# Kernel tuning notes

Hardware: AMD Instinct MI355X
Metric: run time of the kernel (lower is better)

## Reference

```python
import jax, jax.numpy as jnp
import numpy as np

N, E, IN, H, OUT, G = 100000, 1600000, 9, 64, 6, 1024
EPS = 1e-5


def setup_inputs() -> dict:
    key = jax.random.key(0)
    ks = jax.random.split(key, 24)
    inp = {
        "x": jax.random.normal(ks[0], (N, IN), dtype=jnp.float32),
        "edge_index": jax.random.randint(ks[1], (2, E), 0, N, dtype=jnp.int64),
        "edge_weight": jax.random.uniform(ks[2], (E,), dtype=jnp.float32),
        "batch": jnp.sort(jax.random.randint(ks[3], (N,), 0, G, dtype=jnp.int64)),
    }
    def lin(k, fan_in, fan_out):
        return jax.random.normal(k, (fan_in, fan_out), dtype=jnp.float32) / np.sqrt(fan_in)
    # GraphConv layer 0: IN -> H; layers 1,2: H -> H
    inp["W_rel0"], inp["W_root0"], inp["b0"] = lin(ks[4], IN, H), lin(ks[5], IN, H), jnp.zeros((H,), jnp.float32)
    inp["W_rel1"], inp["W_root1"], inp["b1"] = lin(ks[6], H, H), lin(ks[7], H, H), jnp.zeros((H,), jnp.float32)
    inp["W_rel2"], inp["W_root2"], inp["b2"] = lin(ks[8], H, H), lin(ks[9], H, H), jnp.zeros((H,), jnp.float32)
    # BatchNorm params for the first num_layers-1 = 2 layers
    inp["g0"], inp["be0"] = jnp.ones((H,), jnp.float32), jnp.zeros((H,), jnp.float32)
    inp["g1"], inp["be1"] = jnp.ones((H,), jnp.float32), jnp.zeros((H,), jnp.float32)
    # MLP head
    inp["W_l1"], inp["b_l1"] = lin(ks[10], H, H), jnp.zeros((H,), jnp.float32)
    inp["W_l2"], inp["b_l2"] = lin(ks[11], H, OUT), jnp.zeros((OUT,), jnp.float32)
    return inp


def graph_conv(x, src, dst, ew, W_rel, W_root, b):
    # PyG GraphConv: out = aggr_add(e_ji * x_j) @ W_rel + b + x @ W_root
    msg = x[src] * ew[:, None]                      # [E, F] gather
    agg = jax.ops.segment_sum(msg, dst, num_segments=x.shape[0])  # [N, F] scatter-add
    return agg @ W_rel + b + x @ W_root


def batch_norm(x, g, b):
    m = jnp.mean(x, axis=0)
    v = jnp.var(x, axis=0)
    return (x - m) * jax.lax.rsqrt(v + EPS) * g + b


def reference(x, edge_index, edge_weight, batch,
              W_rel0, W_root0, b0, W_rel1, W_root1, b1, W_rel2, W_root2, b2,
              g0, be0, g1, be1, W_l1, b_l1, W_l2, b_l2):
    src, dst = edge_index[0], edge_index[1]
    # layer 0: conv -> BN -> relu (dropout p applied only in training; eval here)
    h = graph_conv(x, src, dst, edge_weight, W_rel0, W_root0, b0)
    h = jax.nn.relu(batch_norm(h, g0, be0))
    # layer 1
    h = graph_conv(h, src, dst, edge_weight, W_rel1, W_root1, b1)
    h = jax.nn.relu(batch_norm(h, g1, be1))
    # layer 2 (no norm/relu)
    h = graph_conv(h, src, dst, edge_weight, W_rel2, W_root2, b2)
    # global mean pool over graphs
    summed = jax.ops.segment_sum(h, batch, num_segments=G)            # [G, H]
    counts = jax.ops.segment_sum(jnp.ones((h.shape[0],), h.dtype), batch, num_segments=G)
    pooled = summed / jnp.maximum(counts, 1.0)[:, None]
    # MLP head
    z = jax.nn.relu(pooled @ W_l1 + b_l1)
    return z @ W_l2 + b_l2
```

## Files before the change

kernel.cpp:

```cpp
#include <hip/hip_runtime.h>
#include <hip/hip_fp16.h>

constexpr int N    = 100000;
constexpr int E    = 1600000;
constexpr int FIN  = 9;
constexpr int OUTF = 6;
constexpr int G    = 1024;
constexpr int NPB  = 256;
constexpr int NB   = (N + NPB - 1) / NPB;
constexpr int CH   = 2048;
constexpr int NCH  = (E + CH - 1) / CH;
constexpr int BCAP = 4864;
constexpr int CBCAP= BCAP + NPB + 8;
constexpr int EBUF = 5888;
constexpr int ZCNT = 256 + G * 64;

typedef _Float16 f16x8 __attribute__((ext_vector_type(8)));
typedef float    f32x4 __attribute__((ext_vector_type(4)));

__device__ __forceinline__ void atomAddF(float* p, float v) { unsafeAtomicAdd(p, v); }

__global__ __launch_bounds__(256) void initK(int* __restrict__ cursor, float* __restrict__ zeros,
    const float* __restrict__ x, __half* __restrict__ x9)
{
    int i = blockIdx.x * 256 + threadIdx.x;
    if (i < NB) cursor[i] = i * BCAP;
    if (i < ZCNT) zeros[i] = 0.f;
    if (i < N * FIN) x9[i] = __float2half(x[i]);
}

__global__ __launch_bounds__(256) void passA(const int* __restrict__ src, const int* __restrict__ dst,
    const float* __restrict__ ew, int* __restrict__ cursor, int2* __restrict__ bucketed)
{
    __shared__ int h[NB];
    __shared__ int hb[NB];
    int t = threadIdx.x;
    for (int i = t; i < NB; i += 256) h[i] = 0;
    __syncthreads();
    int base = blockIdx.x * CH;
    int myS[8], myD[8], rk[8]; float myW[8];
#pragma unroll
    for (int i = 0; i < 8; i++) {
        int e = base + i * 256 + t;
        if (e < E) {
            myS[i] = src[e]; myD[i] = dst[e]; myW[i] = ew[e];
            rk[i] = atomicAdd(&h[myD[i] >> 8], 1);
        } else myD[i] = -1;
    }
    __syncthreads();
    for (int i = t; i < NB; i += 256) hb[i] = h[i] ? atomicAdd(&cursor[i], h[i]) : 0;
    __syncthreads();
#pragma unroll
    for (int i = 0; i < 8; i++) if (myD[i] >= 0) {
        int packed = myS[i] | ((myD[i] & 255) << 24);
        bucketed[hb[myD[i] >> 8] + rk[i]] = make_int2(packed, __float_as_int(myW[i]));
    }
}

__global__ __launch_bounds__(NPB) void passB(const int* __restrict__ cursor,
    const int2* __restrict__ bucketed, int* __restrict__ ebeg, int* __restrict__ eend,
    int2* __restrict__ csr)
{
    __shared__ int2 ebuf[EBUF];
    __shared__ int cl[NPB], sa[NPB], sb[NPB], curs[NPB];
    int b = blockIdx.x, t = threadIdx.x;
    int node0 = b * NPB;
    int nnode = min(NPB, N - node0);
    int cnt = cursor[b] - b * BCAP;
    int abase = b * BCAP;
    int base = b * CBCAP;
    bool fits = (cnt <= EBUF);
    cl[t] = 0;
    __syncthreads();
    for (int e = t; e < cnt; e += NPB) {
        int2 r = bucketed[abase + e];
        if (fits) ebuf[e] = r;
        atomicAdd(&cl[((unsigned)r.x) >> 24], 1);
    }
    __syncthreads();
    int deg = cl[t];
    int pc = (deg + 1) & ~1;
    int* cur = sa; int* nxt = sb;
    cur[t] = pc;
    __syncthreads();
    for (int o = 1; o < NPB; o <<= 1) {
        int v = cur[t];
        if (t >= o) v += cur[t - o];
        nxt[t] = v;
        __syncthreads();
        int* tmp = cur; cur = nxt; nxt = tmp;
    }
    int off = cur[t] - pc;
    if (t < nnode) { ebeg[node0 + t] = base + off; eend[node0 + t] = base + off + deg; }
    curs[t] = off;
    __syncthreads();
    for (int e = t; e < cnt; e += NPB) {
        int2 r = fits ? ebuf[e] : bucketed[abase + e];
        int dl = ((unsigned)r.x) >> 24;
        int pos = base + atomicAdd(&curs[dl], 1);
        csr[pos] = make_int2(r.x & 0x00FFFFFF, r.y);
    }
    __syncthreads();
    if (t < nnode && (deg & 1)) csr[base + off + deg] = make_int2(0, 0);
    if (t < 4) csr[base + cur[NPB - 1] + t] = make_int2(0, 0);
}

__global__ __launch_bounds__(256) void wprep(const float* __restrict__ Wrel1, const float* __restrict__ Wroot1,
    const float* __restrict__ Wrel2, const float* __restrict__ Wroot2, __half* __restrict__ Wt)
{
    int i = blockIdx.x * 256 + threadIdx.x;
    int layer = i >> 13, r = i & 8191;
    int c = r >> 6, k = r & 63;
    const float* Wrel = layer ? Wrel2 : Wrel1;
    const float* Wroot = layer ? Wroot2 : Wroot1;
    float v = (c < 64) ? Wrel[k * 64 + c] : Wroot[k * 64 + (c - 64)];
    Wt[i] = __float2half(v);
}

__global__ __launch_bounds__(256) void gather9(const __half* __restrict__ x9,
    const int2* __restrict__ csr, const int* __restrict__ ebeg, const int* __restrict__ eend,
    float* __restrict__ agg9)
{
    int t = threadIdx.x, lane = t & 63;
    int es = lane >> 4, fc = min(lane & 15, FIN - 1);
    int wv = (blockIdx.x * blockDim.x + t) >> 6;
    int nw = (gridDim.x * blockDim.x) >> 6;
    for (int n = wv; n < N; n += nw) {
        int beg = ebeg[n], end = eend[n];
        int last = end - 1;
        int2 eA0 = csr[min(beg + es,      last)];
        int2 eB0 = csr[min(beg + 4 + es,  last)];
        int2 eA1 = csr[min(beg + 8 + es,  last)];
        int2 eB1 = csr[min(beg + 12 + es, last)];
        __half xA = x9[(size_t)eA0.x * FIN + fc];
        __half xB = x9[(size_t)eB0.x * FIN + fc];
        float a0 = 0.f, a1 = 0.f;
        for (int k = beg; k < end; k += 8) {
            int2 eA2 = csr[min(k + 16 + es, last)];
            int2 eB2 = csr[min(k + 20 + es, last)];
            __half nxA = x9[(size_t)eA1.x * FIN + fc];
            __half nxB = x9[(size_t)eB1.x * FIN + fc];
            float wA = (k + es     < end) ? __int_as_float(eA0.y) : 0.f;
            float wB = (k + 4 + es < end) ? __int_as_float(eB0.y) : 0.f;
            a0 = fmaf(wA, __half2float(xA), a0);
            a1 = fmaf(wB, __half2float(xB), a1);
            eA0 = eA1; eB0 = eB1; eA1 = eA2; eB1 = eB2;
            xA = nxA; xB = nxB;
        }
        float r = a0 + a1;
        r += __shfl(r, lane ^ 16, 64);
        r += __shfl(r, lane ^ 32, 64);
        if (lane < FIN) agg9[(size_t)n * FIN + lane] = r;
    }
}

__global__ __launch_bounds__(256) void proj0post(const float* __restrict__ x,
    const float* __restrict__ agg9, const float* __restrict__ Wrel,
    const float* __restrict__ Wroot, const float* __restrict__ bias,
    __half* __restrict__ H0, float* __restrict__ stats)
{
    int t = threadIdx.x, j = t & 63;
    int nl = __builtin_amdgcn_readfirstlane(t >> 6);
    float wrel[FIN], wroot[FIN];
#pragma unroll
    for (int k = 0; k < FIN; k++) { wrel[k] = Wrel[k * 64 + j]; wroot[k] = Wroot[k * 64 + j]; }
    float bj = bias[j];
    float s1 = 0.f, s2 = 0.f;
    const int ntiles = N / 4;
    for (int tile = blockIdx.x; tile < ntiles; tile += gridDim.x) {
        int n = tile * 4 + nl;
        const float* xr = x + (size_t)n * FIN;
        const float* ar = agg9 + (size_t)n * FIN;
        float acc = bj;
#pragma unroll
        for (int k = 0; k < FIN; k++) {
            acc = fmaf(ar[k], wrel[k], acc);
            acc = fmaf(xr[k], wroot[k], acc);
        }
        H0[(size_t)n * 64 + j] = __float2half(acc);
        s1 += acc; s2 += acc * acc;
    }
    __shared__ float sred[256];
    sred[t] = s1; __syncthreads();
    if (t < 64) atomAddF(&stats[t], sred[t] + sred[t+64] + sred[t+128] + sred[t+192]);
    __syncthreads();
    sred[t] = s2; __syncthreads();
    if (t < 64) atomAddF(&stats[64 + t], sred[t] + sred[t+64] + sred[t+128] + sred[t+192]);
}

__global__ __launch_bounds__(256) void projm(const __half* __restrict__ Hin, const __half* __restrict__ Wt,
    const float* __restrict__ bias, const float* __restrict__ stats,
    const float* __restrict__ gam, const float* __restrict__ bet,
    __half* __restrict__ P, __half* __restrict__ Hout)
{
    int t = threadIdx.x, lane = t & 63;
    int wv = blockIdx.x * 4 + (t >> 6);
    int nw = gridDim.x * 4;
    int n16 = lane & 15, quad = lane >> 4;
    constexpr float invN = 1.0f / (float)N;
    float sc[16], sh[16];
#pragma unroll
    for (int jj = 0; jj < 16; jj++) {
        int k = (jj < 8) ? (quad * 8 + jj) : (32 + quad * 8 + (jj - 8));
        float m = stats[k] * invN;
        float v = stats[64 + k] * invN - m * m;
        sc[jj] = gam[k] * rsqrtf(v + 1e-5f);
        sh[jj] = bet[k] - m * sc[jj];
    }
    f16x8 bf[8][2];
#pragma unroll
    for (int ct = 0; ct < 8; ct++)
#pragma unroll
        for (int kh = 0; kh < 2; kh++)
            bf[ct][kh] = *(const f16x8*)(Wt + (size_t)(ct * 16 + n16) * 64 + kh * 32 + quad * 8);
    float bcol[4];
#pragma unroll
    for (int i = 0; i < 4; i++) bcol[i] = bias[i * 16 + n16];
    const int NT = N / 16;
    for (int tile = wv; tile < NT; tile += nw) {
        int n0 = tile * 16;
        f16x8 r0 = *(const f16x8*)(Hin + (size_t)(n0 + n16) * 64 + quad * 8);
        f16x8 r1 = *(const f16x8*)(Hin + (size_t)(n0 + n16) * 64 + 32 + quad * 8);
        f16x8 a0, a1;
#pragma unroll
        for (int jj = 0; jj < 8; jj++) {
            a0[jj] = (_Float16)fmaxf(fmaf((float)r0[jj], sc[jj],     sh[jj]),     0.f);
            a1[jj] = (_Float16)fmaxf(fmaf((float)r1[jj], sc[jj + 8], sh[jj + 8]), 0.f);
        }
        f32x4 acc[8];
#pragma unroll
        for (int ct = 0; ct < 8; ct++) {
            f32x4 c = {0.f, 0.f, 0.f, 0.f};
            c = __builtin_amdgcn_mfma_f32_16x16x32_f16(a0, bf[ct][0], c, 0, 0, 0);
            c = __builtin_amdgcn_mfma_f32_16x16x32_f16(a1, bf[ct][1], c, 0, 0, 0);
            acc[ct] = c;
        }
#pragma unroll
        for (int ct = 0; ct < 8; ct++) {
#pragma unroll
            for (int r = 0; r < 4; r++) {
                int n = n0 + quad * 4 + r;
                if (ct < 4) P[(size_t)n * 64 + ct * 16 + n16] = __float2half(acc[ct][r]);
                else Hout[(size_t)n * 64 + (ct - 4) * 16 + n16] = __float2half(acc[ct][r] + bcol[ct - 4]);
            }
        }
    }
}

template<int EPI>
__global__ __launch_bounds__(256) void gather(const __half* __restrict__ P, __half* H,
    const int2* __restrict__ csr, const int* __restrict__ ebeg, const int* __restrict__ eend,
    float* __restrict__ stats, const int* __restrict__ batch, float* __restrict__ pool)
{
    int t = threadIdx.x, lane = t & 63;
    int wv = (blockIdx.x * blockDim.x + t) >> 6;
    int nw = (gridDim.x * blockDim.x) >> 6;
    float s1 = 0.f, s2 = 0.f;
    const int NPAIR = N / 2;
    for (int pr = wv; pr < NPAIR; pr += nw) {
        int n0 = 2 * pr, n1 = n0 + 1;
        int b0 = ebeg[n0], m0 = (eend[n0] - b0 + 1) >> 1;
        int b1 = ebeg[n1], m1 = (eend[n1] - b1 + 1) >> 1;
        const int4* q0 = (const int4*)csr + (b0 >> 1);
        const int4* q1 = (const int4*)csr + (b1 >> 1);
        int c0 = max(m0 - 1, 0), c1 = max(m1 - 1, 0);
        float x0 = __half2float(H[(size_t)n0 * 64 + lane]);
        float x1 = __half2float(H[(size_t)n1 * 64 + lane]);
        int4 qaA = q0[0],           qbA = q0[min(1, c0)];
        int4 qcA = q1[0],           qdA = q1[min(1, c1)];
        int4 qaB = q0[min(2, c0)],  qbB = q0[min(3, c0)];
        int4 qcB = q1[min(2, c1)],  qdB = q1[min(3, c1)];
        __half pa0 = P[(size_t)qaA.x * 64 + lane], pa1 = P[(size_t)qaA.z * 64 + lane];
        __half pb0 = P[(size_t)qbA.x * 64 + lane], pb1 = P[(size_t)qbA.z * 64 + lane];
        __half pc0 = P[(size_t)qcA.x * 64 + lane], pc1 = P[(size_t)qcA.z * 64 + lane];
        __half pd0 = P[(size_t)qdA.x * 64 + lane], pd1 = P[(size_t)qdA.z * 64 + lane];
        float a0 = 0.f, a1 = 0.f, a2 = 0.f, a3 = 0.f;
        float a4 = 0.f, a5 = 0.f, a6 = 0.f, a7 = 0.f;
        int mm = max(m0, m1);
        for (int k = 0; k < mm; k += 2) {
            int4 qaC = q0[min(k + 4, c0)], qbC = q0[min(k + 5, c0)];
            int4 qcC = q1[min(k + 4, c1)], qdC = q1[min(k + 5, c1)];
            __half na0 = P[(size_t)qaB.x * 64 + lane], na1 = P[(size_t)qaB.z * 64 + lane];
            __half nb0 = P[(size_t)qbB.x * 64 + lane], nb1 = P[(size_t)qbB.z * 64 + lane];
            __half nc0 = P[(size_t)qcB.x * 64 + lane], nc1 = P[(size_t)qcB.z * 64 + lane];
            __half nd0 = P[(size_t)qdB.x * 64 + lane], nd1 = P[(size_t)qdB.z * 64 + lane];
            float wa = (k     < m0) ? __int_as_float(qaA.y) : 0.f;
            float wA = (k     < m0) ? __int_as_float(qaA.w) : 0.f;
            float wb = (k + 1 < m0) ? __int_as_float(qbA.y) : 0.f;
            float wB = (k + 1 < m0) ? __int_as_float(qbA.w) : 0.f;
            float wc = (k     < m1) ? __int_as_float(qcA.y) : 0.f;
            float wC = (k     < m1) ? __int_as_float(qcA.w) : 0.f;
            float wd = (k + 1 < m1) ? __int_as_float(qdA.y) : 0.f;
            float wD = (k + 1 < m1) ? __int_as_float(qdA.w) : 0.f;
            a0 = fmaf(wa, __half2float(pa0), a0); a1 = fmaf(wA, __half2float(pa1), a1);
            a2 = fmaf(wb, __half2float(pb0), a2); a3 = fmaf(wB, __half2float(pb1), a3);
            a4 = fmaf(wc, __half2float(pc0), a4); a5 = fmaf(wC, __half2float(pc1), a5);
            a6 = fmaf(wd, __half2float(pd0), a6); a7 = fmaf(wD, __half2float(pd1), a7);
            qaA = qaB; qbA = qbB; qcA = qcB; qdA = qdB;
            qaB = qaC; qbB = qbC; qcB = qcC; qdB = qdC;
            pa0 = na0; pa1 = na1; pb0 = nb0; pb1 = nb1;
            pc0 = nc0; pc1 = nc1; pd0 = nd0; pd1 = nd1;
        }
        float r0 = x0 + ((a0 + a2) + (a1 + a3));
        float r1 = x1 + ((a4 + a6) + (a5 + a7));
        if constexpr (EPI == 0) {
            H[(size_t)n0 * 64 + lane] = __float2half(r0);
            H[(size_t)n1 * 64 + lane] = __float2half(r1);
            s1 += r0 + r1; s2 += r0 * r0 + r1 * r1;
        } else {
            atomAddF(&pool[batch[n0] * 64 + lane], r0);
            atomAddF(&pool[batch[n1] * 64 + lane], r1);
        }
    }
    if constexpr (EPI == 0) {
        __shared__ float sred[256];
        sred[t] = s1; __syncthreads();
        if (t < 64) atomAddF(&stats[t], sred[t] + sred[t+64] + sred[t+128] + sred[t+192]);
        __syncthreads();
        sred[t] = s2; __syncthreads();
        if (t < 64) atomAddF(&stats[64 + t], sred[t] + sred[t+64] + sred[t+128] + sred[t+192]);
    }
}

__global__ __launch_bounds__(64) void head(const float* __restrict__ pool,
    const int* __restrict__ batch, const float* __restrict__ Wl1, const float* __restrict__ bl1,
    const float* __restrict__ Wl2, const float* __restrict__ bl2, float* __restrict__ out)
{
    int g = blockIdx.x, t = threadIdx.x;
    __shared__ float sp[64];
    __shared__ float sz[64];
    __shared__ int scnt;
    if (t == 0) {
        int lo = 0, hi = N;
        while (lo < hi) { int m = (lo + hi) >> 1; if (batch[m] < g) lo = m + 1; else hi = m; }
        int lo2 = lo, hi2 = N;
        while (lo2 < hi2) { int m = (lo2 + hi2) >> 1; if (batch[m] < g + 1) lo2 = m + 1; else hi2 = m; }
        scnt = lo2 - lo;
    }
    __syncthreads();
    float cnt = fmaxf((float)scnt, 1.0f);
    sp[t] = pool[g * 64 + t] / cnt;
    __syncthreads();
    float acc = bl1[t];
#pragma unroll
    for (int k = 0; k < 64; k++) acc = fmaf(sp[k], Wl1[k * 64 + t], acc);
    sz[t] = fmaxf(acc, 0.f);
    __syncthreads();
    if (t < OUTF) {
        float o = bl2[t];
#pragma unroll
        for (int k = 0; k < 64; k++) o = fmaf(sz[k], Wl2[k * OUTF + t], o);
        out[g * OUTF + t] = o;
    }
}

extern "C" void kernel_launch(void* const* d_in, const int* in_sizes, int n_in,
                              void* d_out, int out_size, void* d_ws, size_t ws_size,
                              hipStream_t stream)
{
    const float* x     = (const float*)d_in[0];
    const int*   ei    = (const int*)d_in[1];
    const float* ew    = (const float*)d_in[2];
    const int*   batch = (const int*)d_in[3];
    const float* Wrel0 = (const float*)d_in[4];
    const float* Wroot0= (const float*)d_in[5];
    const float* b0    = (const float*)d_in[6];
    const float* Wrel1 = (const float*)d_in[7];
    const float* Wroot1= (const float*)d_in[8];
    const float* b1    = (const float*)d_in[9];
    const float* Wrel2 = (const float*)d_in[10];
    const float* Wroot2= (const float*)d_in[11];
    const float* b2    = (const float*)d_in[12];
    const float* g0    = (const float*)d_in[13];
    const float* be0   = (const float*)d_in[14];
    const float* g1    = (const float*)d_in[15];
    const float* be1   = (const float*)d_in[16];
    const float* Wl1   = (const float*)d_in[17];
    const float* bl1   = (const float*)d_in[18];
    const float* Wl2   = (const float*)d_in[19];
    const float* bl2   = (const float*)d_in[20];
    const int* srcI = ei;
    const int* dstI = ei + E;

    __half* Ha     = (__half*)d_ws;
    __half* Hb     = Ha + (size_t)N * 64;
    __half* P      = Hb + (size_t)N * 64;
    int2*   csr    = (int2*)(P + (size_t)N * 64);
    int*    ebeg   = (int*)(csr + (size_t)NB * CBCAP);
    int*    eend   = ebeg + N;
    int*    cursor = eend + N;
    float*  stats0 = (float*)(cursor + NB);
    float*  stats1 = stats0 + 128;
    float*  pool   = stats1 + 128;
    __half* Wt1    = (__half*)(pool + G * 64);
    __half* Wt2    = Wt1 + 128 * 64;
    float*  agg9   = (float*)(Wt2 + 128 * 64);
    __half* x9     = (__half*)(agg9 + (size_t)N * FIN);
    int2*   bucketed = (int2*)Ha;

    initK<<<(N * FIN + 255) / 256, 256, 0, stream>>>(cursor, stats0, x, x9);
    passA<<<NCH, 256, 0, stream>>>(srcI, dstI, ew, cursor, bucketed);
    passB<<<NB, NPB, 0, stream>>>(cursor, bucketed, ebeg, eend, csr);
    wprep<<<64, 256, 0, stream>>>(Wrel1, Wroot1, Wrel2, Wroot2, Wt1);

    gather9<<<2048, 256, 0, stream>>>(x9, csr, ebeg, eend, agg9);
    proj0post<<<2048, 256, 0, stream>>>(x, agg9, Wrel0, Wroot0, b0, Ha, stats0);

    projm<<<1024, 256, 0, stream>>>(Ha, Wt1, b1, stats0, g0, be0, P, Hb);
    gather<0><<<2048, 256, 0, stream>>>(P, Hb, csr, ebeg, eend, stats1, nullptr, nullptr);

    projm<<<1024, 256, 0, stream>>>(Hb, Wt2, b2, stats1, g1, be1, P, Ha);
    gather<1><<<2048, 256, 0, stream>>>(P, Ha, csr, ebeg, eend, nullptr, batch, pool);

    head<<<G, 64, 0, stream>>>(pool, batch, Wl1, bl1, Wl2, bl2, (float*)d_out);
}
```

Before: 479.1 us.

## Replace pull-based CSR gathers with push-based CSC scatter using float atomics

Builds the edge structure keyed by source instead of destination, so each node pushes its weighted features to its neighbours with float atomic adds into zeroed fp32 accumulators. A separate fin kernel then adds the root term and computes BN stats or the pool. This removes the random per-edge row gathers of P, but adds 1.6M×64 atomics per layer, an extra zeroing pass over two N×64 fp32 buffers, and an extra read/write pass per layer. Accumulation order becomes nondeterministic.

```diff
diff --git a/kernel.cpp b/kernel.cpp
--- a/kernel.cpp
+++ b/kernel.cpp
@@ -21,15 +21,21 @@
 __device__ __forceinline__ void atomAddF(float* p, float v) { unsafeAtomicAdd(p, v); }
 
 __global__ __launch_bounds__(256) void initK(int* __restrict__ cursor, float* __restrict__ zeros,
-    const float* __restrict__ x, __half* __restrict__ x9)
+    float* __restrict__ agg9)
 {
     int i = blockIdx.x * 256 + threadIdx.x;
     if (i < NB) cursor[i] = i * BCAP;
     if (i < ZCNT) zeros[i] = 0.f;
-    if (i < N * FIN) x9[i] = __float2half(x[i]);
-}
-
-__global__ __launch_bounds__(256) void passA(const int* __restrict__ src, const int* __restrict__ dst,
+    if (i < N * FIN) agg9[i] = 0.f;
+}
+
+__global__ __launch_bounds__(256) void zeroK(f32x4* __restrict__ z)
+{
+    size_t i = (size_t)blockIdx.x * 256 + threadIdx.x;
+    if (i < (size_t)2 * N * 64 / 4) z[i] = f32x4{0.f, 0.f, 0.f, 0.f};
+}
+
+__global__ __launch_bounds__(256) void passA(const int* __restrict__ pay, const int* __restrict__ key,
     const float* __restrict__ ew, int* __restrict__ cursor, int2* __restrict__ bucketed)
 {
     __shared__ int h[NB];
@@ -43,7 +49,7 @@
     for (int i = 0; i < 8; i++) {
         int e = base + i * 256 + t;
         if (e < E) {
-            myS[i] = src[e]; myD[i] = dst[e]; myW[i] = ew[e];
+            myS[i] = pay[e]; myD[i] = key[e]; myW[i] = ew[e];
             rk[i] = atomicAdd(&h[myD[i] >> 8], 1);
         } else myD[i] = -1;
     }
@@ -117,40 +123,28 @@
     Wt[i] = __float2half(v);
 }
 
-__global__ __launch_bounds__(256) void gather9(const __half* __restrict__ x9,
-    const int2* __restrict__ csr, const int* __restrict__ ebeg, const int* __restrict__ eend,
+__global__ __launch_bounds__(256) void scatter9(const float* __restrict__ x,
+    const int2* __restrict__ csc, const int* __restrict__ ebeg, const int* __restrict__ eend,
     float* __restrict__ agg9)
 {
     int t = threadIdx.x, lane = t & 63;
-    int es = lane >> 4, fc = min(lane & 15, FIN - 1);
+    int e = lane / 9;
+    int f = lane - e * 9;
+    bool elane = (e < 7);
     int wv = (blockIdx.x * blockDim.x + t) >> 6;
     int nw = (gridDim.x * blockDim.x) >> 6;
     for (int n = wv; n < N; n += nw) {
         int beg = ebeg[n], end = eend[n];
+        if (beg >= end) continue;
+        float xf = x[(size_t)n * FIN + f];
         int last = end - 1;
-        int2 eA0 = csr[min(beg + es,      last)];
-        int2 eB0 = csr[min(beg + 4 + es,  last)];
-        int2 eA1 = csr[min(beg + 8 + es,  last)];
-        int2 eB1 = csr[min(beg + 12 + es, last)];
-        __half xA = x9[(size_t)eA0.x * FIN + fc];
-        __half xB = x9[(size_t)eB0.x * FIN + fc];
-        float a0 = 0.f, a1 = 0.f;
-        for (int k = beg; k < end; k += 8) {
-            int2 eA2 = csr[min(k + 16 + es, last)];
-            int2 eB2 = csr[min(k + 20 + es, last)];
-            __half nxA = x9[(size_t)eA1.x * FIN + fc];
-            __half nxB = x9[(size_t)eB1.x * FIN + fc];
-            float wA = (k + es     < end) ? __int_as_float(eA0.y) : 0.f;
-            float wB = (k + 4 + es < end) ? __int_as_float(eB0.y) : 0.f;
-            a0 = fmaf(wA, __half2float(xA), a0);
-            a1 = fmaf(wB, __half2float(xB), a1);
-            eA0 = eA1; eB0 = eB1; eA1 = eA2; eB1 = eB2;
-            xA = nxA; xB = nxB;
-        }
-        float r = a0 + a1;
-        r += __shfl(r, lane ^ 16, 64);
-        r += __shfl(r, lane ^ 32, 64);
-        if (lane < FIN) agg9[(size_t)n * FIN + lane] = r;
+        for (int k = beg; k < end; k += 7) {
+            int idx = k + e;
+            int2 q = csc[min(idx, last)];
+            float w = __int_as_float(q.y);
+            if (elane && idx < end && w != 0.f)
+                atomAddF(&agg9[(size_t)q.x * FIN + f], w * xf);
+        }
     }
 }
 
@@ -247,69 +241,52 @@
     }
 }
 
-template<int EPI>
-__global__ __launch_bounds__(256) void gather(const __half* __restrict__ P, __half* H,
-    const int2* __restrict__ csr, const int* __restrict__ ebeg, const int* __restrict__ eend,
-    float* __restrict__ stats, const int* __restrict__ batch, float* __restrict__ pool)
+__global__ __launch_bounds__(256) void scatterN(const __half* __restrict__ P,
+    const int2* __restrict__ csc, const int* __restrict__ ebeg, const int* __restrict__ eend,
+    float* __restrict__ agg)
 {
     int t = threadIdx.x, lane = t & 63;
     int wv = (blockIdx.x * blockDim.x + t) >> 6;
     int nw = (gridDim.x * blockDim.x) >> 6;
+    for (int n = wv; n < N; n += nw) {
+        int beg = ebeg[n], end = eend[n];
+        int npk = (end - beg + 1) >> 1;
+        if (npk <= 0) continue;
+        float p = __half2float(P[(size_t)n * 64 + lane]);
+        const int4* q4 = (const int4*)csc + (beg >> 1);
+        int c = npk - 1;
+        int4 qa = q4[0];
+        int4 qb = q4[min(1, c)];
+        for (int k = 0; k < npk; k++) {
+            int4 qn = q4[min(k + 2, c)];
+            int d0 = __builtin_amdgcn_readfirstlane(qa.x);
+            int w0 = __builtin_amdgcn_readfirstlane(qa.y);
+            int d1 = __builtin_amdgcn_readfirstlane(qa.z);
+            int w1 = __builtin_amdgcn_readfirstlane(qa.w);
+            if (w0) atomAddF(&agg[(size_t)d0 * 64 + lane], __int_as_float(w0) * p);
+            if (w1 && k * 2 + 1 < end - beg)
+                atomAddF(&agg[(size_t)d1 * 64 + lane], __int_as_float(w1) * p);
+            qa = qb; qb = qn;
+        }
+    }
+}
+
+template<int EPI>
+__global__ __launch_bounds__(256) void fin(const float* __restrict__ agg, __half* __restrict__ H,
+    float* __restrict__ stats, const int* __restrict__ batch, float* __restrict__ pool)
+{
+    int t = threadIdx.x, j = t & 63;
+    int nl = __builtin_amdgcn_readfirstlane(t >> 6);
     float s1 = 0.f, s2 = 0.f;
-    const int NPAIR = N / 2;
-    for (int pr = wv; pr < NPAIR; pr += nw) {
-        int n0 = 2 * pr, n1 = n0 + 1;
-        int b0 = ebeg[n0], m0 = (eend[n0] - b0 + 1) >> 1;
-        int b1 = ebeg[n1], m1 = (eend[n1] - b1 + 1) >> 1;
-        const int4* q0 = (const int4*)csr + (b0 >> 1);
-        const int4* q1 = (const int4*)csr + (b1 >> 1);
-        int c0 = max(m0 - 1, 0), c1 = max(m1 - 1, 0);
-        float x0 = __half2float(H[(size_t)n0 * 64 + lane]);
-        float x1 = __half2float(H[(size_t)n1 * 64 + lane]);
-        int4 qaA = q0[0],           qbA = q0[min(1, c0)];
-        int4 qcA = q1[0],           qdA = q1[min(1, c1)];
-        int4 qaB = q0[min(2, c0)],  qbB = q0[min(3, c0)];
-        int4 qcB = q1[min(2, c1)],  qdB = q1[min(3, c1)];
-        __half pa0 = P[(size_t)qaA.x * 64 + lane], pa1 = P[(size_t)qaA.z * 64 + lane];
-        __half pb0 = P[(size_t)qbA.x * 64 + lane], pb1 = P[(size_t)qbA.z * 64 + lane];
-        __half pc0 = P[(size_t)qcA.x * 64 + lane], pc1 = P[(size_t)qcA.z * 64 + lane];
-        __half pd0 = P[(size_t)qdA.x * 64 + lane], pd1 = P[(size_t)qdA.z * 64 + lane];
-        float a0 = 0.f, a1 = 0.f, a2 = 0.f, a3 = 0.f;
-        float a4 = 0.f, a5 = 0.f, a6 = 0.f, a7 = 0.f;
-        int mm = max(m0, m1);
-        for (int k = 0; k < mm; k += 2) {
-            int4 qaC = q0[min(k + 4, c0)], qbC = q0[min(k + 5, c0)];
-            int4 qcC = q1[min(k + 4, c1)], qdC = q1[min(k + 5, c1)];
-            __half na0 = P[(size_t)qaB.x * 64 + lane], na1 = P[(size_t)qaB.z * 64 + lane];
-            __half nb0 = P[(size_t)qbB.x * 64 + lane], nb1 = P[(size_t)qbB.z * 64 + lane];
-            __half nc0 = P[(size_t)qcB.x * 64 + lane], nc1 = P[(size_t)qcB.z * 64 + lane];
-            __half nd0 = P[(size_t)qdB.x * 64 + lane], nd1 = P[(size_t)qdB.z * 64 + lane];
-            float wa = (k     < m0) ? __int_as_float(qaA.y) : 0.f;
-            float wA = (k     < m0) ? __int_as_float(qaA.w) : 0.f;
-            float wb = (k + 1 < m0) ? __int_as_float(qbA.y) : 0.f;
-            float wB = (k + 1 < m0) ? __int_as_float(qbA.w) : 0.f;
-            float wc = (k     < m1) ? __int_as_float(qcA.y) : 0.f;
-            float wC = (k     < m1) ? __int_as_float(qcA.w) : 0.f;
-            float wd = (k + 1 < m1) ? __int_as_float(qdA.y) : 0.f;
-            float wD = (k + 1 < m1) ? __int_as_float(qdA.w) : 0.f;
-            a0 = fmaf(wa, __half2float(pa0), a0); a1 = fmaf(wA, __half2float(pa1), a1);
-            a2 = fmaf(wb, __half2float(pb0), a2); a3 = fmaf(wB, __half2float(pb1), a3);
-            a4 = fmaf(wc, __half2float(pc0), a4); a5 = fmaf(wC, __half2float(pc1), a5);
-            a6 = fmaf(wd, __half2float(pd0), a6); a7 = fmaf(wD, __half2float(pd1), a7);
-            qaA = qaB; qbA = qbB; qcA = qcB; qdA = qdB;
-            qaB = qaC; qbB = qbC; qcB = qcC; qdB = qdC;
-            pa0 = na0; pa1 = na1; pb0 = nb0; pb1 = nb1;
-            pc0 = nc0; pc1 = nc1; pd0 = nd0; pd1 = nd1;
-        }
-        float r0 = x0 + ((a0 + a2) + (a1 + a3));
-        float r1 = x1 + ((a4 + a6) + (a5 + a7));
+    const int ntiles = N / 4;
+    for (int tile = blockIdx.x; tile < ntiles; tile += gridDim.x) {
+        int n = tile * 4 + nl;
+        float r = __half2float(H[(size_t)n * 64 + j]) + agg[(size_t)n * 64 + j];
         if constexpr (EPI == 0) {
-            H[(size_t)n0 * 64 + lane] = __float2half(r0);
-            H[(size_t)n1 * 64 + lane] = __float2half(r1);
-            s1 += r0 + r1; s2 += r0 * r0 + r1 * r1;
+            H[(size_t)n * 64 + j] = __float2half(r);
+            s1 += r; s2 += r * r;
         } else {
-            atomAddF(&pool[batch[n0] * 64 + lane], r0);
-            atomAddF(&pool[batch[n1] * 64 + lane], r1);
+            atomAddF(&pool[batch[n] * 64 + j], r);
         }
     }
     if constexpr (EPI == 0) {
@@ -385,8 +362,8 @@
     __half* Ha     = (__half*)d_ws;
     __half* Hb     = Ha + (size_t)N * 64;
     __half* P      = Hb + (size_t)N * 64;
-    int2*   csr    = (int2*)(P + (size_t)N * 64);
-    int*    ebeg   = (int*)(csr + (size_t)NB * CBCAP);
+    int2*   csc    = (int2*)(P + (size_t)N * 64);
+    int*    ebeg   = (int*)(csc + (size_t)NB * CBCAP);
     int*    eend   = ebeg + N;
     int*    cursor = eend + N;
     float*  stats0 = (float*)(cursor + NB);
@@ -395,22 +372,26 @@
     __half* Wt1    = (__half*)(pool + G * 64);
     __half* Wt2    = Wt1 + 128 * 64;
     float*  agg9   = (float*)(Wt2 + 128 * 64);
-    __half* x9     = (__half*)(agg9 + (size_t)N * FIN);
-    int2*   bucketed = (int2*)Ha;
-
-    initK<<<(N * FIN + 255) / 256, 256, 0, stream>>>(cursor, stats0, x, x9);
-    passA<<<NCH, 256, 0, stream>>>(srcI, dstI, ew, cursor, bucketed);
-    passB<<<NB, NPB, 0, stream>>>(cursor, bucketed, ebeg, eend, csr);
+    float*  aggA   = agg9 + (size_t)N * FIN;
+    float*  aggB   = aggA + (size_t)N * 64;
+    int2*   bucketed = (int2*)aggA;
+
+    initK<<<(N * FIN + 255) / 256, 256, 0, stream>>>(cursor, stats0, agg9);
+    passA<<<NCH, 256, 0, stream>>>(dstI, srcI, ew, cursor, bucketed);
+    passB<<<NB, NPB, 0, stream>>>(cursor, bucketed, ebeg, eend, csc);
+    zeroK<<<(2 * N * 64 / 4 + 255) / 256, 256, 0, stream>>>((f32x4*)aggA);
     wprep<<<64, 256, 0, stream>>>(Wrel1, Wroot1, Wrel2, Wroot2, Wt1);
 
-    gather9<<<2048, 256, 0, stream>>>(x9, csr, ebeg, eend, agg9);
+    scatter9<<<2048, 256, 0, stream>>>(x, csc, ebeg, eend, agg9);
     proj0post<<<2048, 256, 0, stream>>>(x, agg9, Wrel0, Wroot0, b0, Ha, stats0);
 
     projm<<<1024, 256, 0, stream>>>(Ha, Wt1, b1, stats0, g0, be0, P, Hb);
-    gather<0><<<2048, 256, 0, stream>>>(P, Hb, csr, ebeg, eend, stats1, nullptr, nullptr);
+    scatterN<<<2048, 256, 0, stream>>>(P, csc, ebeg, eend, aggA);
+    fin<0><<<2048, 256, 0, stream>>>(aggA, Hb, stats1, nullptr, nullptr);
 
     projm<<<1024, 256, 0, stream>>>(Hb, Wt2, b2, stats1, g1, be1, P, Ha);
-    gather<1><<<2048, 256, 0, stream>>>(P, Ha, csr, ebeg, eend, nullptr, batch, pool);
+    scatterN<<<2048, 256, 0, stream>>>(P, csc, ebeg, eend, aggB);
+    fin<1><<<2048, 256, 0, stream>>>(aggB, Ha, nullptr, batch, pool);
 
     head<<<G, 64, 0, stream>>>(pool, batch, Wl1, bl1, Wl2, bl2, (float*)d_out);
 }
```

Result: slower. 1.297 ms (+170.7%).

## Gather 4 features per lane across 4 edges with shuffle reduction

Applied to the files above, without the earlier changes.

Restructures the gather kernel so each wave handles one node. Each lane loads 8 bytes (4 half features) of a neighbour row, and four groups of 16 lanes work on different edges at once, replacing one 2-byte load per lane per edge. Partial sums are combined across the edge groups with cross-lane shuffles, and only one quarter of the lanes write the output and the BN statistics. The aim is fewer, wider memory transactions per edge, at the cost of shuffle overhead, lanes idle on low-degree nodes, and one node per wave instead of two.

```diff
diff --git a/kernel.cpp b/kernel.cpp
--- a/kernel.cpp
+++ b/kernel.cpp
@@ -253,72 +253,75 @@
     float* __restrict__ stats, const int* __restrict__ batch, float* __restrict__ pool)
 {
     int t = threadIdx.x, lane = t & 63;
+    int f4 = lane & 15;
+    int es = lane >> 4;
     int wv = (blockIdx.x * blockDim.x + t) >> 6;
     int nw = (gridDim.x * blockDim.x) >> 6;
-    float s1 = 0.f, s2 = 0.f;
-    const int NPAIR = N / 2;
-    for (int pr = wv; pr < NPAIR; pr += nw) {
-        int n0 = 2 * pr, n1 = n0 + 1;
-        int b0 = ebeg[n0], m0 = (eend[n0] - b0 + 1) >> 1;
-        int b1 = ebeg[n1], m1 = (eend[n1] - b1 + 1) >> 1;
-        const int4* q0 = (const int4*)csr + (b0 >> 1);
-        const int4* q1 = (const int4*)csr + (b1 >> 1);
-        int c0 = max(m0 - 1, 0), c1 = max(m1 - 1, 0);
-        float x0 = __half2float(H[(size_t)n0 * 64 + lane]);
-        float x1 = __half2float(H[(size_t)n1 * 64 + lane]);
-        int4 qaA = q0[0],           qbA = q0[min(1, c0)];
-        int4 qcA = q1[0],           qdA = q1[min(1, c1)];
-        int4 qaB = q0[min(2, c0)],  qbB = q0[min(3, c0)];
-        int4 qcB = q1[min(2, c1)],  qdB = q1[min(3, c1)];
-        __half pa0 = P[(size_t)qaA.x * 64 + lane], pa1 = P[(size_t)qaA.z * 64 + lane];
-        __half pb0 = P[(size_t)qbA.x * 64 + lane], pb1 = P[(size_t)qbA.z * 64 + lane];
-        __half pc0 = P[(size_t)qcA.x * 64 + lane], pc1 = P[(size_t)qcA.z * 64 + lane];
-        __half pd0 = P[(size_t)qdA.x * 64 + lane], pd1 = P[(size_t)qdA.z * 64 + lane];
+    const uint2* Pr = (const uint2*)P;
+    float s1v[4] = {0.f, 0.f, 0.f, 0.f}, s2v[4] = {0.f, 0.f, 0.f, 0.f};
+    for (int n = wv; n < N; n += nw) {
+        int beg = ebeg[n], end = eend[n];
         float a0 = 0.f, a1 = 0.f, a2 = 0.f, a3 = 0.f;
-        float a4 = 0.f, a5 = 0.f, a6 = 0.f, a7 = 0.f;
-        int mm = max(m0, m1);
-        for (int k = 0; k < mm; k += 2) {
-            int4 qaC = q0[min(k + 4, c0)], qbC = q0[min(k + 5, c0)];
-            int4 qcC = q1[min(k + 4, c1)], qdC = q1[min(k + 5, c1)];
-            __half na0 = P[(size_t)qaB.x * 64 + lane], na1 = P[(size_t)qaB.z * 64 + lane];
-            __half nb0 = P[(size_t)qbB.x * 64 + lane], nb1 = P[(size_t)qbB.z * 64 + lane];
-            __half nc0 = P[(size_t)qcB.x * 64 + lane], nc1 = P[(size_t)qcB.z * 64 + lane];
-            __half nd0 = P[(size_t)qdB.x * 64 + lane], nd1 = P[(size_t)qdB.z * 64 + lane];
-            float wa = (k     < m0) ? __int_as_float(qaA.y) : 0.f;
-            float wA = (k     < m0) ? __int_as_float(qaA.w) : 0.f;
-            float wb = (k + 1 < m0) ? __int_as_float(qbA.y) : 0.f;
-            float wB = (k + 1 < m0) ? __int_as_float(qbA.w) : 0.f;
-            float wc = (k     < m1) ? __int_as_float(qcA.y) : 0.f;
-            float wC = (k     < m1) ? __int_as_float(qcA.w) : 0.f;
-            float wd = (k + 1 < m1) ? __int_as_float(qdA.y) : 0.f;
-            float wD = (k + 1 < m1) ? __int_as_float(qdA.w) : 0.f;
-            a0 = fmaf(wa, __half2float(pa0), a0); a1 = fmaf(wA, __half2float(pa1), a1);
-            a2 = fmaf(wb, __half2float(pb0), a2); a3 = fmaf(wB, __half2float(pb1), a3);
-            a4 = fmaf(wc, __half2float(pc0), a4); a5 = fmaf(wC, __half2float(pc1), a5);
-            a6 = fmaf(wd, __half2float(pd0), a6); a7 = fmaf(wD, __half2float(pd1), a7);
-            qaA = qaB; qbA = qbB; qcA = qcB; qdA = qdB;
-            qaB = qaC; qbB = qbC; qcB = qcC; qdB = qdC;
-            pa0 = na0; pa1 = na1; pb0 = nb0; pb1 = nb1;
-            pc0 = nc0; pc1 = nc1; pd0 = nd0; pd1 = nd1;
-        }
-        float r0 = x0 + ((a0 + a2) + (a1 + a3));
-        float r1 = x1 + ((a4 + a6) + (a5 + a7));
-        if constexpr (EPI == 0) {
-            H[(size_t)n0 * 64 + lane] = __float2half(r0);
-            H[(size_t)n1 * 64 + lane] = __float2half(r1);
-            s1 += r0 + r1; s2 += r0 * r0 + r1 * r1;
-        } else {
-            atomAddF(&pool[batch[n0] * 64 + lane], r0);
-            atomAddF(&pool[batch[n1] * 64 + lane], r1);
+        if (beg < end) {
+            int last = end - 1;
+            int2 qA = csr[min(beg + es,     last)];
+            int2 qB = csr[min(beg + 4 + es, last)];
+            uint2 pA = Pr[(size_t)qA.x * 16 + f4];
+            for (int k = beg; k < end; k += 4) {
+                int2 qC = csr[min(k + 8 + es, last)];
+                uint2 pB = Pr[(size_t)qB.x * 16 + f4];
+                float w = (k + es < end) ? __int_as_float(qA.y) : 0.f;
+                float2 p01 = __half22float2(__builtin_bit_cast(__half2, pA.x));
+                float2 p23 = __half22float2(__builtin_bit_cast(__half2, pA.y));
+                a0 = fmaf(w, p01.x, a0);
+                a1 = fmaf(w, p01.y, a1);
+                a2 = fmaf(w, p23.x, a2);
+                a3 = fmaf(w, p23.y, a3);
+                qA = qB; qB = qC; pA = pB;
+            }
+        }
+        a0 += __shfl_xor(a0, 16, 64); a1 += __shfl_xor(a1, 16, 64);
+        a2 += __shfl_xor(a2, 16, 64); a3 += __shfl_xor(a3, 16, 64);
+        a0 += __shfl_xor(a0, 32, 64); a1 += __shfl_xor(a1, 32, 64);
+        a2 += __shfl_xor(a2, 32, 64); a3 += __shfl_xor(a3, 32, 64);
+        if (es == 0) {
+            uint2 hx = ((const uint2*)H)[(size_t)n * 16 + f4];
+            float2 h01 = __half22float2(__builtin_bit_cast(__half2, hx.x));
+            float2 h23 = __half22float2(__builtin_bit_cast(__half2, hx.y));
+            float r0 = h01.x + a0, r1 = h01.y + a1;
+            float r2 = h23.x + a2, r3 = h23.y + a3;
+            if constexpr (EPI == 0) {
+                uint2 o;
+                o.x = __builtin_bit_cast(unsigned, __floats2half2_rn(r0, r1));
+                o.y = __builtin_bit_cast(unsigned, __floats2half2_rn(r2, r3));
+                ((uint2*)H)[(size_t)n * 16 + f4] = o;
+                s1v[0] += r0; s1v[1] += r1; s1v[2] += r2; s1v[3] += r3;
+                s2v[0] += r0 * r0; s2v[1] += r1 * r1; s2v[2] += r2 * r2; s2v[3] += r3 * r3;
+            } else {
+                int b = batch[n];
+                atomAddF(&pool[b * 64 + f4 * 4 + 0], r0);
+                atomAddF(&pool[b * 64 + f4 * 4 + 1], r1);
+                atomAddF(&pool[b * 64 + f4 * 4 + 2], r2);
+                atomAddF(&pool[b * 64 + f4 * 4 + 3], r3);
+            }
         }
     }
     if constexpr (EPI == 0) {
-        __shared__ float sred[256];
-        sred[t] = s1; __syncthreads();
-        if (t < 64) atomAddF(&stats[t], sred[t] + sred[t+64] + sred[t+128] + sred[t+192]);
+        __shared__ float red[4][64];
+        int wi = t >> 6;
+        if (es == 0) {
+#pragma unroll
+            for (int i = 0; i < 4; i++) red[wi][f4 * 4 + i] = s1v[i];
+        }
         __syncthreads();
-        sred[t] = s2; __syncthreads();
-        if (t < 64) atomAddF(&stats[64 + t], sred[t] + sred[t+64] + sred[t+128] + sred[t+192]);
+        if (t < 64) atomAddF(&stats[t], red[0][t] + red[1][t] + red[2][t] + red[3][t]);
+        __syncthreads();
+        if (es == 0) {
+#pragma unroll
+            for (int i = 0; i < 4; i++) red[wi][f4 * 4 + i] = s2v[i];
+        }
+        __syncthreads();
+        if (t < 64) atomAddF(&stats[64 + t], red[0][t] + red[1][t] + red[2][t] + red[3][t]);
     }
 }
 
```

Result: slower. 546.5 us (+14.1%).
